# Performance work log

Measured on AMD Instinct MI355X. Metric: run time of the kernel, lower is better.

## Reference

```python
import jax, jax.numpy as jnp
import numpy as np

N_NODES = 10000
N_EDGES = 128000


def _edge_conv(x, row, col, edge_attr, w1, b1, w2, b2):
    # gather endpoints, concat edge features, 2-layer MLP per edge
    m = jnp.concatenate([x[row], x[col], edge_attr], axis=1)  # [E, 2*in+edge]
    m = jax.nn.relu(m @ w1 + b1) @ w2 + b2                    # [E, out]
    # scatter-mean onto source nodes (flow='target_to_source' -> aggregate on row)
    n = x.shape[0]
    s = jax.ops.segment_sum(m, row, num_segments=n)
    cnt = jax.ops.segment_sum(jnp.ones((row.shape[0], 1), m.dtype), row, num_segments=n)
    out = s / jnp.maximum(cnt, 1.0)
    return out, m


def setup_inputs() -> dict:
    key = jax.random.key(0)
    ks = jax.random.split(key, 24)
    f = jnp.float32

    def lin(kw, kb, fan_in, fan_out):
        lim = 1.0 / np.sqrt(fan_in)
        w = jax.random.uniform(kw, (fan_in, fan_out), f, -lim, lim)
        b = jax.random.uniform(kb, (fan_out,), f, -lim, lim)
        return w, b

    inp = {}
    inp['x_org'] = jax.random.normal(ks[0], (N_NODES, 256), f)
    inp['x_rot'] = jax.random.normal(ks[1], (N_NODES, 4), f)
    inp['edge_index'] = jax.random.randint(ks[2], (2, N_EDGES), 0, N_NODES, jnp.int64 if jax.config.jax_enable_x64 else jnp.int32)
    inp['edge_attr'] = jax.random.normal(ks[3], (N_EDGES, 640), f)
    inp['edge_rot'] = jax.random.normal(ks[4], (N_EDGES, 4), f)

    # conv1: Linear(2*260+644=1164, 64), Linear(64, 64)
    inp['c1_w1'], inp['c1_b1'] = lin(ks[5], ks[6], 1164, 64)
    inp['c1_w2'], inp['c1_b2'] = lin(ks[7], ks[8], 64, 64)
    # conv2: Linear(2*64+704=832, 64), Linear(64, 64)
    inp['c2_w1'], inp['c2_b1'] = lin(ks[9], ks[10], 832, 64)
    inp['c2_w2'], inp['c2_b2'] = lin(ks[11], ks[12], 64, 64)
    # conv3: Linear(2*128+128=384, 64), Linear(64, 64)
    inp['c3_w1'], inp['c3_b1'] = lin(ks[13], ks[14], 384, 64)
    inp['c3_w2'], inp['c3_b2'] = lin(ks[15], ks[16], 64, 64)
    # conv4: Linear(384, 64), Linear(64, 64)
    inp['c4_w1'], inp['c4_b1'] = lin(ks[17], ks[18], 384, 64)
    inp['c4_w2'], inp['c4_b2'] = lin(ks[19], ks[20], 64, 64)
    # lin1: Linear(64, 4)
    inp['lin1_w'], inp['lin1_b'] = lin(ks[21], ks[22], 64, 4)
    # edge_fc: Linear(64, 32) -> ReLU -> Linear(32, 1)
    k23 = jax.random.split(ks[23], 4)
    inp['efc_w1'], inp['efc_b1'] = lin(k23[0], k23[1], 64, 32)
    inp['efc_w2'], inp['efc_b2'] = lin(k23[2], k23[3], 32, 1)
    return inp


def reference(x_org, x_rot, edge_index, edge_attr, edge_rot,
              c1_w1, c1_b1, c1_w2, c1_b2,
              c2_w1, c2_b1, c2_w2, c2_b2,
              c3_w1, c3_b1, c3_w2, c3_b2,
              c4_w1, c4_b1, c4_w2, c4_b2,
              lin1_w, lin1_b, efc_w1, efc_b1, efc_w2, efc_b2):
    node_feat = jnp.concatenate([x_org, x_rot], axis=1)
    edge_feat = jnp.concatenate([edge_attr, edge_rot], axis=1)
    row, col = edge_index[0], edge_index[1]
    E = edge_index.shape[1]

    x1, edge_x1 = _edge_conv(node_feat, row, col, edge_feat, c1_w1, c1_b1, c1_w2, c1_b2)
    edge_x1 = jax.nn.relu(edge_x1)

    x2, edge_x2 = _edge_conv(x1, row, col, jnp.concatenate([edge_attr, edge_x1], axis=1),
                             c2_w1, c2_b1, c2_w2, c2_b2)
    x2 = jax.nn.relu(x2)
    edge_x2 = jax.nn.relu(edge_x2)

    x3, edge_x3 = _edge_conv(jnp.concatenate([x2, x1], axis=1), row, col,
                             jnp.concatenate([edge_x2, edge_x1], axis=1),
                             c3_w1, c3_b1, c3_w2, c3_b2)
    x3 = jax.nn.relu(x3)
    edge_x3 = jax.nn.relu(edge_x3)

    x4, edge_x4 = _edge_conv(jnp.concatenate([x3, x2], axis=1), row, col,
                             jnp.concatenate([edge_x3, edge_x2], axis=1),
                             c4_w1, c4_b1, c4_w2, c4_b2)
    x4 = jax.nn.relu(x4)

    x = x4 @ lin1_w + lin1_b  # [N, 4]
    h = edge_x4[: E // 2] + edge_x4[E // 2:]
    pred_edge_res = jax.nn.relu(h @ efc_w1 + efc_b1) @ efc_w2 + efc_b2  # [E/2, 1]

    # F.normalize(x, p=2, dim=1)
    x = x / jnp.maximum(jnp.linalg.norm(x, axis=1, keepdims=True), 1e-12)
    return x, pred_edge_res
```

## Files before the change

### kernel.cpp

```cpp
#include <hip/hip_runtime.h>
#include <stdint.h>


#define N_NODES 10000
#define N_EDGES 128000
#define E_HALF  64000
#define NBLK    1000

typedef unsigned short u16;

using bf16x8 = __attribute__((ext_vector_type(8))) short;
using f32x4  = __attribute__((ext_vector_type(4))) float;

#define MFMA16(A, B, C) C = __builtin_amdgcn_mfma_f32_16x16x32_bf16(A, B, C, 0, 0, 0)

__device__ __align__(256) float g_acc[N_NODES * 64];
__device__ __align__(256) float g_deg[N_NODES];
__device__ __align__(256) float g_P[N_NODES * 128];
__device__ __align__(256) float g_x1[N_NODES * 64];
__device__ __align__(256) float g_x2[N_NODES * 64];
__device__ __align__(256) float g_x3[N_NODES * 64];
__device__ __align__(256) u16  g_fragA[(size_t)NBLK * 16384];
__device__ __align__(256) u16  g_fragB[(size_t)NBLK * 16384];
__device__ __align__(256) float g_Q2 [(size_t)N_EDGES * 64];
__device__ __align__(256) float g_ex4[(size_t)N_EDGES * 64];
__device__ __align__(256) u16  g_wpA_hi[2 * 4096];
__device__ __align__(256) u16  g_wpA_lo[2 * 4096];
__device__ __align__(256) u16  g_wp2_hi[4096];
__device__ __align__(256) u16  g_wp2_lo[4096];
__device__ __align__(256) u16  g_wnp_hi[4 * 8192];
__device__ __align__(256) u16  g_wnp_lo[4 * 8192];
__device__ __align__(256) u16  g_wpC_hi[10 * 8192];
__device__ __align__(256) u16  g_wpC_lo[10 * 8192];
__device__ __align__(256) int g_row[N_EDGES];
__device__ __align__(256) int g_col[N_EDGES];
__device__ int g_mode;
__device__ int g_is64;

__device__ __forceinline__ float b2f(u16 u) {
    return __uint_as_float(((unsigned int)u) << 16);
}
__device__ __forceinline__ u16 f2b(float f) {
    unsigned int u = __float_as_uint(f);
    u += 0x7FFFu + ((u >> 16) & 1u);
    return (u16)(u >> 16);
}
__device__ __forceinline__ float ldf(const u16* p)   { return b2f(*p); }
__device__ __forceinline__ float ldf(const float* p) { return *p; }
__device__ __forceinline__ void  stf(u16* p, float v)   { *p = f2b(v); }
__device__ __forceinline__ void  stf(float* p, float v) { *p = v; }

__device__ __forceinline__ float4 load4(const float* p) { return *(const float4*)p; }
__device__ __forceinline__ float4 load4(const u16* p) {
    ushort4 v = *(const ushort4*)p;
    return make_float4(b2f(v.x), b2f(v.y), b2f(v.z), b2f(v.w));
}

__device__ __forceinline__ void gl_lds16(const void* g, void* l) {
    __builtin_amdgcn_global_load_lds(
        (const __attribute__((address_space(1))) void*)g,
        (__attribute__((address_space(3))) void*)l, 16, 0, 0);
}

__device__ __forceinline__ void split_pack(float4 v, uint2& hi, uint2& lo) {
    unsigned int ux = __float_as_uint(v.x), uy = __float_as_uint(v.y);
    unsigned int uz = __float_as_uint(v.z), uw = __float_as_uint(v.w);
    unsigned int hx = ux & 0xFFFF0000u, hy = uy & 0xFFFF0000u;
    unsigned int hz = uz & 0xFFFF0000u, hw = uw & 0xFFFF0000u;
    hi.x = (hx >> 16) | hy;
    hi.y = (hz >> 16) | hw;
    u16 lx = f2b(v.x - __uint_as_float(hx));
    u16 ly = f2b(v.y - __uint_as_float(hy));
    u16 lz = f2b(v.z - __uint_as_float(hz));
    u16 lw = f2b(v.w - __uint_as_float(hw));
    lo.x = (unsigned int)lx | ((unsigned int)ly << 16);
    lo.y = (unsigned int)lz | ((unsigned int)lw << 16);
}

__device__ __forceinline__ void mk_frag(float4 v0, float4 v1,
                                        bf16x8& fh, bf16x8& fl) {
    uint2 h0, l0, h1, l1;
    split_pack(v0, h0, l0);
    split_pack(v1, h1, l1);
    union { unsigned int w[4]; bf16x8 v; } H, L;
    H.w[0] = h0.x; H.w[1] = h0.y; H.w[2] = h1.x; H.w[3] = h1.y;
    L.w[0] = l0.x; L.w[1] = l0.y; L.w[2] = l1.x; L.w[3] = l1.y;
    fh = H.v; fl = L.v;
}

__global__ void detect_kernel(const void* x_org_v, const int* __restrict__ eidx) {
    const u16* w = (const u16*)x_org_v;
    const int t = threadIdx.x;
    int ok = 0;
    for (int i = t; i < 128; i += 64) {
        u16 v = w[i];
        int ex = (v >> 7) & 0xFF;
        ok += ((ex >= 0x68 && ex <= 0x88) || ((v & 0x7FFFu) == 0)) ? 1 : 0;
    }
    #pragma unroll
    for (int off = 32; off >= 1; off >>= 1) ok += __shfl_xor(ok, off);
    bool allz = true;
    for (int i = t; i < 2048; i += 64) allz = allz && (eidx[2 * i + 1] == 0);
    unsigned long long m = __ballot(allz);
    if (t == 0) {
        g_mode = (ok >= 110) ? 0 : 1;
        g_is64 = (m == ~0ull) ? 1 : 0;
    }
}

__global__ void cvt_idx(const int* __restrict__ eidx) {
    const int e = blockIdx.x * 256 + threadIdx.x;
    if (g_is64) {
        g_row[e] = eidx[2 * e];
        g_col[e] = eidx[2 * (e + N_EDGES)];
    } else {
        g_row[e] = eidx[e];
        g_col[e] = eidx[e + N_EDGES];
    }
}

__global__ void zero_all() {
    const int i = blockIdx.x * 256 + threadIdx.x;
    g_acc[i] = 0.f;
    if (i < N_NODES) g_deg[i] = 0.f;
}

__global__ void deg_kernel() {
    const int e = blockIdx.x * 256 + threadIdx.x;
    if (e < N_EDGES) atomicAdd(&g_deg[g_row[e]], 1.0f);
}

template<typename TW>
__device__ void pack_w_body(const TW* w1a, const TW* w2, const TW* w1b,
                            int we, int ns, int hioff, int nsn, int nsc) {
    const int idx = blockIdx.x * 256 + threadIdx.x;
    const int t1 = ns * 4096;
    const int t2 = t1 + 4096;
    const int t3 = t2 + nsn * 8192;
    if (idx < t1) {
        const int s = idx >> 12;
        const int rem = idx & 4095;
        const int kt = rem >> 11, ct = (rem >> 9) & 3, l = (rem >> 3) & 63, r = rem & 7;
        const int k = s * 64 + kt * 32 + 4 * (l >> 4) + (r & 3) + 16 * (r >> 2);
        const float v = ldf(w1a + (size_t)(we + k) * 64 + ct * 16 + (l & 15));
        const u16 hh = f2b(v);
        g_wpA_hi[idx] = hh;
        g_wpA_lo[idx] = f2b(v - b2f(hh));
    } else if (idx < t2) {
        const int rem = idx - t1;
        const int kt = rem >> 11, ct = (rem >> 9) & 3, l = (rem >> 3) & 63, r = rem & 7;
        const int k = kt * 32 + 4 * (l >> 4) + (r & 3) + 16 * (r >> 2);
        const float v = ldf(w2 + (size_t)k * 64 + ct * 16 + (l & 15));
        const u16 hh = f2b(v);
        g_wp2_hi[rem] = hh;
        g_wp2_lo[rem] = f2b(v - b2f(hh));
    } else if (idx < t3) {
        const int rem = idx - t2;
        const int s = rem >> 13;
        const int kt = (rem >> 12) & 1, ct = (rem >> 9) & 7, l = (rem >> 3) & 63, r = rem & 7;
        const int k = s * 64 + kt * 32 + 4 * (l >> 4) + (r & 3) + 16 * (r >> 2);
        const int col = ct * 16 + (l & 15);
        const int row = (col < 64) ? k : (hioff + k);
        const float v = ldf(w1a + (size_t)row * 64 + (col & 63));
        const u16 hh = f2b(v);
        g_wnp_hi[rem] = hh;
        g_wnp_lo[rem] = f2b(v - b2f(hh));
    } else if (idx < t3 + nsc * 8192) {
        const int rem = idx - t3;
        const int s = rem >> 13;
        const int kt = (rem >> 12) & 1, ct = (rem >> 9) & 7, l = (rem >> 3) & 63, r = rem & 7;
        const int k = s * 64 + kt * 32 + 4 * (l >> 4) + (r & 3) + 16 * (r >> 2);
        const int col = ct * 16 + (l & 15);
        float v;
        if (col < 64) v = ldf(w1a + (size_t)(520 + k) * 64 + col);
        else          v = ldf(w1b + (size_t)(128 + k) * 64 + (col - 64));
        const u16 hh = f2b(v);
        g_wpC_hi[rem] = hh;
        g_wpC_lo[rem] = f2b(v - b2f(hh));
    }
}
__global__ void pack_w_k(const void* w1a, const void* w2, const void* w1b,
                         int we, int ns, int hioff, int nsn, int nsc) {
    if (g_mode == 0)
        pack_w_body<u16>((const u16*)w1a, (const u16*)w2, (const u16*)w1b,
                         we, ns, hioff, nsn, nsc);
    else
        pack_w_body<float>((const float*)w1a, (const float*)w2, (const float*)w1b,
                         we, ns, hioff, nsn, nsc);
}

template<typename TA, int NS1, int NS2, bool TAIL>
__device__ void node_mfma_body(float* smrot, float* smwt,
        const TA* A1, const float* A2, const TA* rotsrc, const TA* w1, float* P) {
    constexpr int NS = NS1 + NS2;
    const int t = threadIdx.x;
    const int lane = t & 63, wid = t >> 6;
    const int q = lane >> 4, n = lane & 15;
    const int r0b = blockIdx.x * 64;

    if constexpr (TAIL) {
        if (t < 64) {
            const int rr = min(r0b + t, N_NODES - 1);
            float4 v = load4(rotsrc + (size_t)rr * 4);
            smrot[t * 4 + 0] = v.x; smrot[t * 4 + 1] = v.y;
            smrot[t * 4 + 2] = v.z; smrot[t * 4 + 3] = v.w;
        }
        for (int i = t; i < 512; i += 256) {
            const int j = i >> 7, c = i & 127;
            const int row = (c < 64) ? (256 + j) : (516 + j);
            smwt[i] = ldf(w1 + (size_t)row * 64 + (c & 63));
        }
        __syncthreads();
    }

    const int arow = min(r0b + wid * 16 + n, N_NODES - 1);

    f32x4 acc[8];
    #pragma unroll
    for (int ct = 0; ct < 8; ++ct) acc[ct] = (f32x4){0.f, 0.f, 0.f, 0.f};

    #pragma unroll
    for (int s = 0; s < NS; ++s) {
        #pragma unroll
        for (int kt = 0; kt < 2; ++kt) {
            float4 v0, v1;
            if (s < NS1) {
                const TA* p = A1 + (size_t)arow * (NS1 * 64) + s * 64 + kt * 32 + q * 4;
                v0 = load4(p); v1 = load4(p + 16);
            } else {
                const float* p = A2 + (size_t)arow * (NS2 * 64) + (s - NS1) * 64
                               + kt * 32 + q * 4;
                v0 = load4(p); v1 = load4(p + 16);
            }
            bf16x8 ah, al;
            mk_frag(v0, v1, ah, al);
            const u16* wph = g_wnp_hi + s * 8192;
            const u16* wpl = g_wnp_lo + s * 8192;
            #pragma unroll
            for (int ct = 0; ct < 8; ++ct) {
                bf16x8 bh = *(const bf16x8*)&wph[(kt * 8 + ct) * 512 + lane * 8];
                bf16x8 bl = *(const bf16x8*)&wpl[(kt * 8 + ct) * 512 + lane * 8];
                MFMA16(ah, bh, acc[ct]);
                MFMA16(al, bh, acc[ct]);
                MFMA16(ah, bl, acc[ct]);
            }
        }
    }

    #pragma unroll
    for (int ct = 0; ct < 8; ++ct) {
        #pragma unroll
        for (int i = 0; i < 4; ++i) {
            const int rl = wid * 16 + 4 * q + i;
            const int row = r0b + rl;
            const int col = ct * 16 + n;
            float v = acc[ct][i];
            if constexpr (TAIL)
                v += smrot[rl * 4 + 0] * smwt[0 * 128 + col]
                   + smrot[rl * 4 + 1] * smwt[1 * 128 + col]
                   + smrot[rl * 4 + 2] * smwt[2 * 128 + col]
                   + smrot[rl * 4 + 3] * smwt[3 * 128 + col];
            if (row < N_NODES) P[(size_t)row * 128 + col] = v;
        }
    }
}

template<int NS1, bool TAIL>
__global__ void __launch_bounds__(256) node_mfma_in(
        const void* A1, const void* rotsrc, const void* w1, float* __restrict__ P) {
    __shared__ float smrot[256], smwt[512];
    if (g_mode == 0)
        node_mfma_body<u16, NS1, 0, TAIL>(smrot, smwt, (const u16*)A1,
            nullptr, (const u16*)rotsrc, (const u16*)w1, P);
    else
        node_mfma_body<float, NS1, 0, TAIL>(smrot, smwt, (const float*)A1,
            nullptr, (const float*)rotsrc, (const float*)w1, P);
}

template<int NS1, int NS2>
__global__ void __launch_bounds__(256) node_mfma_ws(
        const float* A1, const float* A2, float* __restrict__ P) {
    __shared__ float smrot[256], smwt[512];
    node_mfma_body<float, NS1, NS2, false>(smrot, smwt, A1, A2,
        (const float*)nullptr, (const float*)nullptr, P);
}

__device__ __forceinline__ void frag_store_o(u16* hreg, int wid, int lane,
        const f32x4 (&oacc)[2][4], u16* Fdst, int blkid) {
    const int q = lane >> 4, n = lane & 15;
    #pragma unroll
    for (int rt = 0; rt < 2; ++rt)
        #pragma unroll
        for (int ct = 0; ct < 4; ++ct)
            #pragma unroll
            for (int i = 0; i < 4; ++i) {
                float v = fmaxf(oacc[rt][ct][i], 0.f);
                unsigned int hb = __float_as_uint(v) & 0xFFFF0000u;
                const u16 hh = (u16)(hb >> 16);
                const u16 hl = f2b(v - __uint_as_float(hb));
                const int off = wid * 4096
                              + (((ct >> 1) * 2 + rt) * 64 + (n >> 2) * 16 + 4 * q + i) * 8
                              + (ct & 1) * 4 + (n & 3);
                hreg[off]        = hh;
                hreg[off + 2048] = hl;
            }
    #pragma unroll
    for (int kt = 0; kt < 2; ++kt)
        #pragma unroll
        for (int rtl = 0; rtl < 2; ++rtl) {
            const int src = wid * 4096 + ((kt * 2 + rtl) * 64 + lane) * 8;
            bf16x8 h8 = *(const bf16x8*)&hreg[src];
            bf16x8 l8 = *(const bf16x8*)&hreg[src + 2048];
            const size_t gb = (size_t)blkid * 16384
                            + (size_t)(kt * 8 + wid * 2 + rtl) * 512 + lane * 8;
            *(bf16x8*)&Fdst[gb]        = h8;
            *(bf16x8*)&Fdst[gb + 8192] = l8;
        }
}

template<typename TA, typename TW>
__device__ void edge_c1_body(u16* smW, int* srow, int* scol,
        float* b1s, float* b2s, float* rot, float* wtl,
        const TA* efa, const TA* rotsrc,
        const TW* w1, const TW* b1v, const TW* b2v) {
    const int t = threadIdx.x;
    const int lane = t & 63, wid = t >> 6;
    const int q = lane >> 4, n = lane & 15;
    const int e0 = blockIdx.x * 128;

    if (t < 128) srow[t] = g_row[e0 + t];
    else         scol[t - 128] = g_col[e0 + t - 128];
    if (t >= 128 && t < 192) b1s[t - 128] = ldf(b1v + (t - 128));
    if (t >= 192)            b2s[t - 192] = ldf(b2v + (t - 192));
    if (t < 128) {
        float4 r4 = load4(rotsrc + (size_t)(e0 + t) * 4);
        rot[t * 4 + 0] = r4.x; rot[t * 4 + 1] = r4.y;
        rot[t * 4 + 2] = r4.z; rot[t * 4 + 3] = r4.w;
    }
    wtl[t] = ldf(w1 + (size_t)(1160 + (t >> 6)) * 64 + (t & 63));

    const TA* arow0 = efa + (size_t)(e0 + wid * 32 + n) * 640;
    const TA* arow1 = efa + (size_t)(e0 + wid * 32 + 16 + n) * 640;

    f32x4 acc[2][8];
    #pragma unroll
    for (int a_ = 0; a_ < 2; ++a_)
        #pragma unroll
        for (int b_ = 0; b_ < 8; ++b_)
            acc[a_][b_] = (f32x4){0.f, 0.f, 0.f, 0.f};

    auto stageW = [&](int s) {
        const char* srch = (const char*)g_wpC_hi + (size_t)s * 16384;
        const char* srcl = (const char*)g_wpC_lo + (size_t)s * 16384;
        char* dsth = (char*)smW + (size_t)(s & 1) * 32768;
        char* dstl = dsth + 16384;
        #pragma unroll
        for (int i = 0; i < 4; ++i) {
            const int off = wid * 4096 + i * 1024;
            gl_lds16(srch + off + lane * 16, dsth + off);
            gl_lds16(srcl + off + lane * 16, dstl + off);
        }
    };
    auto stageW2 = [&]() {
        #pragma unroll
        for (int i = 0; i < 4; ++i) {
            const int L = wid * 4096 + i * 1024;
            const char* src = (L < 8192) ? (const char*)g_wp2_hi + L
// ... 78 lines not shown
                        + g_P[(size_t)srow[rl] * 128 + col]
                        + g_P[(size_t)scol[rl] * 128 + 64 + col]
                        + rot[rl * 4 + 0] * wtl[0 * 64 + col]
                        + rot[rl * 4 + 1] * wtl[1 * 64 + col]
                        + rot[rl * 4 + 2] * wtl[2 * 64 + col]
                        + rot[rl * 4 + 3] * wtl[3 * 64 + col];
                v = fmaxf(v, 0.f);
                unsigned int hb = __float_as_uint(v) & 0xFFFF0000u;
                const u16 hh = (u16)(hb >> 16);
                const u16 hl = f2b(v - __uint_as_float(hb));
                const int off = wid * 4096
                              + (((ct >> 1) * 2 + rt) * 64 + (n >> 2) * 16 + 4 * q + i) * 8
                              + (ct & 1) * 4 + (n & 3);
                hreg[off]        = hh;
                hreg[off + 2048] = hl;
            }

    __builtin_amdgcn_sched_barrier(0);
    asm volatile("s_waitcnt vmcnt(0)");
    __builtin_amdgcn_sched_barrier(0);
    __builtin_amdgcn_s_barrier();

    f32x4 oacc[2][4];
    #pragma unroll
    for (int rt = 0; rt < 2; ++rt)
        #pragma unroll
        for (int ct = 0; ct < 4; ++ct) {
            const float bb = b2s[ct * 16 + n];
            oacc[rt][ct] = (f32x4){bb, bb, bb, bb};
        }
    #pragma unroll
    for (int kt = 0; kt < 2; ++kt) {
        const int r0 = wid * 4096 + ((kt * 2 + 0) * 64 + lane) * 8;
        const int r1 = wid * 4096 + ((kt * 2 + 1) * 64 + lane) * 8;
        bf16x8 ah0 = *(const bf16x8*)&hreg[r0];
        bf16x8 ah1 = *(const bf16x8*)&hreg[r1];
        bf16x8 al0 = *(const bf16x8*)&hreg[r0 + 2048];
        bf16x8 al1 = *(const bf16x8*)&hreg[r1 + 2048];
        #pragma unroll
        for (int ct = 0; ct < 4; ++ct) {
            bf16x8 bh = *(const bf16x8*)&smW[(kt * 4 + ct) * 512 + lane * 8];
            bf16x8 bl = *(const bf16x8*)&smW[4096 + (kt * 4 + ct) * 512 + lane * 8];
            MFMA16(ah0, bh, oacc[0][ct]);
            MFMA16(ah1, bh, oacc[1][ct]);
            MFMA16(al0, bh, oacc[0][ct]);
            MFMA16(al1, bh, oacc[1][ct]);
            MFMA16(ah0, bl, oacc[0][ct]);
            MFMA16(ah1, bl, oacc[1][ct]);
        }
    }

    #pragma unroll
    for (int rt = 0; rt < 2; ++rt)
        #pragma unroll
        for (int ct = 0; ct < 4; ++ct)
            #pragma unroll
            for (int i = 0; i < 4; ++i) {
                const int rl = wid * 32 + rt * 16 + 4 * q + i;
                atomicAdd(&g_acc[(size_t)srow[rl] * 64 + ct * 16 + n], oacc[rt][ct][i]);
            }
    frag_store_o(hreg, wid, lane, oacc, g_fragA, blockIdx.x);
}

__global__ void __launch_bounds__(256, 2) edge_c1(
        const void* efa, const void* rotsrc,
        const void* w1, const void* b1, const void* b2) {
    __shared__ __align__(16) u16 smW[32768];
    __shared__ int srow[128], scol[128];
    __shared__ float b1s[64], b2s[64], rot[512], wtl[256];
    if (g_mode == 0)
        edge_c1_body<u16, u16>(smW, srow, scol, b1s, b2s, rot, wtl,
            (const u16*)efa, (const u16*)rotsrc,
            (const u16*)w1, (const u16*)b1, (const u16*)b2);
    else
        edge_c1_body<float, float>(smW, srow, scol, b1s, b2s, rot, wtl,
            (const float*)efa, (const float*)rotsrc,
            (const float*)w1, (const float*)b1, (const float*)b2);
}

template<typename TW, int NSF, bool HASQ2, bool FRAG_OUT>
__device__ void edge_lite_body(u16* smW, int* srow, int* scol,
        float* b1s, float* b2s,
        const u16* f0, const u16* f1,
        const TW* b1v, const TW* b2v, u16* Ffrag, float* fout) {
    const int t = threadIdx.x;
    const int lane = t & 63, wid = t >> 6;
    const int q = lane >> 4, n = lane & 15;
    const int e0 = blockIdx.x * 128;
    const size_t blkb = (size_t)blockIdx.x * 16384;
    constexpr int N2 = 2 * NSF * 4096;

    #pragma unroll
    for (int i = 0; i < (NSF + 1) * 4; ++i) {
        const int L = wid * ((NSF + 1) * 4096) + i * 1024;
        const char* src;
        if (L < NSF * 8192)                 src = (const char*)g_wpA_hi + L;
        else if (L < 2 * NSF * 8192)        src = (const char*)g_wpA_lo + (L - NSF * 8192);
        else if (L < 2 * NSF * 8192 + 8192) src = (const char*)g_wp2_hi + (L - 2 * NSF * 8192);
        else                                src = (const char*)g_wp2_lo + (L - 2 * NSF * 8192 - 8192);
        gl_lds16(src + lane * 16, (char*)smW + L);
    }

    if (t < 128) srow[t] = g_row[e0 + t];
    else         scol[t - 128] = g_col[e0 + t - 128];
    if (t >= 128 && t < 192) b1s[t - 128] = ldf(b1v + (t - 128));
    if (t >= 192)            b2s[t - 192] = ldf(b2v + (t - 192));
    __syncthreads();

    f32x4 acc[2][4];
    #pragma unroll
    for (int a_ = 0; a_ < 2; ++a_)
        #pragma unroll
        for (int b_ = 0; b_ < 4; ++b_)
            acc[a_][b_] = (f32x4){0.f, 0.f, 0.f, 0.f};

    #pragma unroll
    for (int s = 0; s < NSF; ++s) {
        const u16* fs = (s == 0) ? f0 : f1;
        #pragma unroll
        for (int kt = 0; kt < 2; ++kt) {
            const size_t ba0 = blkb + (size_t)(kt * 8 + wid * 2 + 0) * 512 + lane * 8;
            const size_t ba1 = blkb + (size_t)(kt * 8 + wid * 2 + 1) * 512 + lane * 8;
            bf16x8 ah0 = *(const bf16x8*)&fs[ba0];
            bf16x8 al0 = *(const bf16x8*)&fs[ba0 + 8192];
            bf16x8 ah1 = *(const bf16x8*)&fs[ba1];
            bf16x8 al1 = *(const bf16x8*)&fs[ba1 + 8192];
            #pragma unroll
            for (int ct = 0; ct < 4; ++ct) {
                bf16x8 bh = *(const bf16x8*)&smW[s * 4096 + (kt * 4 + ct) * 512 + lane * 8];
                bf16x8 bl = *(const bf16x8*)&smW[NSF * 4096 + s * 4096 + (kt * 4 + ct) * 512 + lane * 8];
                MFMA16(ah0, bh, acc[0][ct]);
                MFMA16(ah1, bh, acc[1][ct]);
                MFMA16(al0, bh, acc[0][ct]);
                MFMA16(al1, bh, acc[1][ct]);
                MFMA16(ah0, bl, acc[0][ct]);
                MFMA16(ah1, bl, acc[1][ct]);
            }
        }
    }

    __builtin_amdgcn_s_barrier();
    u16* hreg = smW + (NSF == 1 ? 16384 : 0);

    #pragma unroll
    for (int rt = 0; rt < 2; ++rt)
        #pragma unroll
        for (int ct = 0; ct < 4; ++ct)
            #pragma unroll
            for (int i = 0; i < 4; ++i) {
                const int rl = wid * 32 + rt * 16 + 4 * q + i;
                const int col = ct * 16 + n;
                float v = acc[rt][ct][i] + b1s[col]
                        + g_P[(size_t)srow[rl] * 128 + col]
                        + g_P[(size_t)scol[rl] * 128 + 64 + col];
                if constexpr (HASQ2)
                    v += g_Q2[(size_t)(e0 + rl) * 64 + col];
                v = fmaxf(v, 0.f);
                unsigned int hb = __float_as_uint(v) & 0xFFFF0000u;
                const u16 hh = (u16)(hb >> 16);
                const u16 hl = f2b(v - __uint_as_float(hb));
                const int off = wid * 4096
                              + (((ct >> 1) * 2 + rt) * 64 + (n >> 2) * 16 + 4 * q + i) * 8
                              + (ct & 1) * 4 + (n & 3);
                hreg[off]        = hh;
                hreg[off + 2048] = hl;
            }

    f32x4 oacc[2][4];
    #pragma unroll
    for (int rt = 0; rt < 2; ++rt)
        #pragma unroll
        for (int ct = 0; ct < 4; ++ct) {
            const float bb = b2s[ct * 16 + n];
            oacc[rt][ct] = (f32x4){bb, bb, bb, bb};
        }
    #pragma unroll
    for (int kt = 0; kt < 2; ++kt) {
        const int r0 = wid * 4096 + ((kt * 2 + 0) * 64 + lane) * 8;
        const int r1 = wid * 4096 + ((kt * 2 + 1) * 64 + lane) * 8;
        bf16x8 ah0 = *(const bf16x8*)&hreg[r0];
        bf16x8 ah1 = *(const bf16x8*)&hreg[r1];
        bf16x8 al0 = *(const bf16x8*)&hreg[r0 + 2048];
        bf16x8 al1 = *(const bf16x8*)&hreg[r1 + 2048];
        #pragma unroll
        for (int ct = 0; ct < 4; ++ct) {
            bf16x8 bh = *(const bf16x8*)&smW[N2 + (kt * 4 + ct) * 512 + lane * 8];
            bf16x8 bl = *(const bf16x8*)&smW[N2 + 4096 + (kt * 4 + ct) * 512 + lane * 8];
            MFMA16(ah0, bh, oacc[0][ct]);
            MFMA16(ah1, bh, oacc[1][ct]);
            MFMA16(al0, bh, oacc[0][ct]);
            MFMA16(al1, bh, oacc[1][ct]);
            MFMA16(ah0, bl, oacc[0][ct]);
            MFMA16(ah1, bl, oacc[1][ct]);
        }
    }

    #pragma unroll
    for (int rt = 0; rt < 2; ++rt)
        #pragma unroll
        for (int ct = 0; ct < 4; ++ct)
            #pragma unroll
            for (int i = 0; i < 4; ++i) {
                const int rl = wid * 32 + rt * 16 + 4 * q + i;
                const int col = ct * 16 + n;
                const float v = oacc[rt][ct][i];
                atomicAdd(&g_acc[(size_t)srow[rl] * 64 + col], v);
                if constexpr (!FRAG_OUT)
                    fout[(size_t)(e0 + rl) * 64 + col] = v;
            }
    if constexpr (FRAG_OUT)
        frag_store_o(hreg, wid, lane, oacc, Ffrag, blockIdx.x);
}

template<int NSF, bool HASQ2, bool FRAG_OUT>
__global__ void __launch_bounds__(256, 2) edge_lite(
        const u16* f0, const u16* f1, const void* b1, const void* b2,
        u16* Ffrag, float* fout) {
    __shared__ __align__(16) u16 smW[(NSF == 1) ? 32768 : 24576];
    __shared__ int srow[128], scol[128];
    __shared__ float b1s[64], b2s[64];
    if (g_mode == 0)
        edge_lite_body<u16, NSF, HASQ2, FRAG_OUT>(smW, srow, scol, b1s, b2s,
            f0, f1, (const u16*)b1, (const u16*)b2, Ffrag, fout);
    else
        edge_lite_body<float, NSF, HASQ2, FRAG_OUT>(smW, srow, scol, b1s, b2s,
            f0, f1, (const float*)b1, (const float*)b2, Ffrag, fout);
}

template<bool RELU>
__global__ void finalize_k(float* __restrict__ dst) {
    const int idx = blockIdx.x * 256 + threadIdx.x;
    float v = g_acc[idx] / fmaxf(g_deg[idx >> 6], 1.0f);
    g_acc[idx] = 0.f;
    if (RELU) v = fmaxf(v, 0.f);
    dst[idx] = v;
}

template<typename T>
__device__ void final_node_body(const T* w, const T* b, T* out) {
    const int t = threadIdx.x;
    const int lane = t & 63;
    const int n = blockIdx.x * 4 + (t >> 6);
    float inv = 1.0f / fmaxf(g_deg[n], 1.0f);
    float x4 = fmaxf(g_acc[(size_t)n * 64 + lane] * inv, 0.0f);
    float r[4];
    #pragma unroll
    for (int j = 0; j < 4; ++j) {
        float v = x4 * ldf(w + lane * 4 + j);
        #pragma unroll
        for (int off = 32; off >= 1; off >>= 1) v += __shfl_xor(v, off);
        r[j] = v + ldf(b + j);
    }
    float nrm = sqrtf(r[0]*r[0] + r[1]*r[1] + r[2]*r[2] + r[3]*r[3]);
    float dn = fmaxf(nrm, 1e-12f);
    if (lane < 4) stf(out + n * 4 + lane, r[lane] / dn);
}
__global__ void final_node(const void* w, const void* b, void* out) {
    if (g_mode == 0) final_node_body<u16>((const u16*)w, (const u16*)b, (u16*)out);
    else             final_node_body<float>((const float*)w, (const float*)b, (float*)out);
}

template<typename T>
__device__ void edge_head_body(const float* ex4, const T* w1, const T* b1,
                               const T* w2, const T* b2, T* out) {
    __shared__ float lw1[2048];
    __shared__ float lw2[32];
    const int t = threadIdx.x;
    for (int i = t; i < 2048; i += 256) lw1[i] = ldf(w1 + i);
    if (t < 32) lw2[t] = ldf(w2 + t);
    __syncthreads();
    const int e = blockIdx.x * 256 + t;
    float a[32];
    #pragma unroll
    for (int j = 0; j < 32; ++j) a[j] = ldf(b1 + j);
    const float* p0 = ex4 + (size_t)e * 64;
    const float* p1 = ex4 + (size_t)(e + E_HALF) * 64;
    for (int c = 0; c < 64; ++c) {
        float h = p0[c] + p1[c];
        #pragma unroll
        for (int j = 0; j < 32; ++j) a[j] += h * lw1[c * 32 + j];
    }
    float s = ldf(b2);
    #pragma unroll
    for (int j = 0; j < 32; ++j) s += fmaxf(a[j], 0.f) * lw2[j];
    stf(out + e, s);
}
__global__ void __launch_bounds__(256) edge_head(const float* ex4,
        const void* w1, const void* b1, const void* w2, const void* b2,
        void* out) {
    if (g_mode == 0)
        edge_head_body<u16>(ex4, (const u16*)w1, (const u16*)b1,
                            (const u16*)w2, (const u16*)b2, (u16*)out + 40000);
    else
        edge_head_body<float>(ex4, (const float*)w1, (const float*)b1,
                              (const float*)w2, (const float*)b2, (float*)out + 40000);
}

__global__ void sentinel_fill(unsigned int* out, int n_words) {
    int i = blockIdx.x * 256 + threadIdx.x;
    if (i < n_words) out[i] = 0x44794479u;
}

static void* sym_addr(const void* symbol) {
    void* p = nullptr;
    (void)hipGetSymbolAddress(&p, symbol);
    return p;
}

extern "C" void kernel_launch(void* const* d_in, const int* in_sizes, int n_in,
                              void* d_out, int out_size, void* d_ws, size_t ws_size,
                              hipStream_t stream) {
    (void)d_ws; (void)ws_size;
    bool ok = (n_in == 27) && (out_size == 104000)
           && (in_sizes[0] == 2560000) && (in_sizes[2] == 256000)
           && (in_sizes[3] == 81920000) && (in_sizes[5] == 74496)
           && (in_sizes[21] == 256) && (in_sizes[25] == 32);
    if (!ok) {
        sentinel_fill<<<204, 256, 0, stream>>>((unsigned int*)d_out, 52000);
        return;
    }
    const void* x_org     = d_in[0];
    const void* x_rot     = d_in[1];
    const int*  eidx      = (const int*)d_in[2];
    const void* edge_attr = d_in[3];
    const void* edge_rot  = d_in[4];

    float* P   = (float*)sym_addr(HIP_SYMBOL(g_P));
    float* x1  = (float*)sym_addr(HIP_SYMBOL(g_x1));
    float* x2  = (float*)sym_addr(HIP_SYMBOL(g_x2));
    float* x3  = (float*)sym_addr(HIP_SYMBOL(g_x3));
    u16*   fA  = (u16*)sym_addr(HIP_SYMBOL(g_fragA));
    u16*   fB  = (u16*)sym_addr(HIP_SYMBOL(g_fragB));
    float* ex4 = (float*)sym_addr(HIP_SYMBOL(g_ex4));

    detect_kernel<<<1, 64, 0, stream>>>(x_org, eidx);
    cvt_idx<<<500, 256, 0, stream>>>(eidx);
    zero_all<<<2500, 256, 0, stream>>>();
    deg_kernel<<<500, 256, 0, stream>>>();

    pack_w_k<<<464, 256, 0, stream>>>(d_in[5], d_in[7], d_in[9], 0, 0, 260, 4, 10);
    node_mfma_in<4, true><<<157, 256, 0, stream>>>(x_org, x_rot, d_in[5], P);
    edge_c1<<<NBLK, 256, 0, stream>>>(edge_attr, edge_rot, d_in[5], d_in[6], d_in[8]);
    finalize_k<false><<<2500, 256, 0, stream>>>(x1);

    pack_w_k<<<64, 256, 0, stream>>>(d_in[9], d_in[11], d_in[9], 768, 1, 64, 1, 0);
    node_mfma_ws<1, 0><<<157, 256, 0, stream>>>(x1, nullptr, P);
    edge_lite<1, true, true><<<NBLK, 256, 0, stream>>>(
        fA, nullptr, d_in[10], d_in[12], fB, nullptr);
    finalize_k<true><<<2500, 256, 0, stream>>>(x2);

    pack_w_k<<<112, 256, 0, stream>>>(d_in[13], d_in[15], d_in[13], 256, 2, 128, 2, 0);
    node_mfma_ws<1, 1><<<157, 256, 0, stream>>>(x2, x1, P);
    edge_lite<2, false, true><<<NBLK, 256, 0, stream>>>(
        fB, fA, d_in[14], d_in[16], fA, nullptr);
    finalize_k<true><<<2500, 256, 0, stream>>>(x3);

    pack_w_k<<<112, 256, 0, stream>>>(d_in[17], d_in[19], d_in[17], 256, 2, 128, 2, 0);
    node_mfma_ws<1, 1><<<157, 256, 0, stream>>>(x3, x2, P);
    edge_lite<2, false, false><<<NBLK, 256, 0, stream>>>(
        fA, fB, d_in[18], d_in[20], nullptr, ex4);

    final_node<<<2500, 256, 0, stream>>>(d_in[21], d_in[22], d_out);
    edge_head<<<250, 256, 0, stream>>>(ex4, d_in[23], d_in[24], d_in[25], d_in[26],
                                       d_out);
}
```

Baseline: 843.0 us.

## Fuse prologue, weight packing, finalize and tail kernels to cut launch count

Result: faster. 820.0 us (-2.7%).

```diff
diff --git a/kernel.cpp b/kernel.cpp
--- a/kernel.cpp
+++ b/kernel.cpp
@@ -24,12 +24,12 @@
 __device__ __align__(256) u16  g_fragB[(size_t)NBLK * 16384];
 __device__ __align__(256) float g_Q2 [(size_t)N_EDGES * 64];
 __device__ __align__(256) float g_ex4[(size_t)N_EDGES * 64];
-__device__ __align__(256) u16  g_wpA_hi[2 * 4096];
-__device__ __align__(256) u16  g_wpA_lo[2 * 4096];
-__device__ __align__(256) u16  g_wp2_hi[4096];
-__device__ __align__(256) u16  g_wp2_lo[4096];
-__device__ __align__(256) u16  g_wnp_hi[4 * 8192];
-__device__ __align__(256) u16  g_wnp_lo[4 * 8192];
+__device__ __align__(256) u16  g_wpA_hi[5 * 4096];
+__device__ __align__(256) u16  g_wpA_lo[5 * 4096];
+__device__ __align__(256) u16  g_wp2_hi[4 * 4096];
+__device__ __align__(256) u16  g_wp2_lo[4 * 4096];
+__device__ __align__(256) u16  g_wnp_hi[9 * 8192];
+__device__ __align__(256) u16  g_wnp_lo[9 * 8192];
 __device__ __align__(256) u16  g_wpC_hi[10 * 8192];
 __device__ __align__(256) u16  g_wpC_lo[10 * 8192];
 __device__ __align__(256) int g_row[N_EDGES];
@@ -88,130 +88,124 @@
     fh = H.v; fl = L.v;
 }
 
-__global__ void detect_kernel(const void* x_org_v, const int* __restrict__ eidx) {
-    const u16* w = (const u16*)x_org_v;
-    const int t = threadIdx.x;
-    int ok = 0;
-    for (int i = t; i < 128; i += 64) {
-        u16 v = w[i];
-        int ex = (v >> 7) & 0xFF;
-        ok += ((ex >= 0x68 && ex <= 0x88) || ((v & 0x7FFFu) == 0)) ? 1 : 0;
-    }
-    #pragma unroll
-    for (int off = 32; off >= 1; off >>= 1) ok += __shfl_xor(ok, off);
-    bool allz = true;
-    for (int i = t; i < 2048; i += 64) allz = allz && (eidx[2 * i + 1] == 0);
-    unsigned long long m = __ballot(allz);
-    if (t == 0) {
-        g_mode = (ok >= 110) ? 0 : 1;
-        g_is64 = (m == ~0ull) ? 1 : 0;
-    }
-}
-
-__global__ void cvt_idx(const int* __restrict__ eidx) {
-    const int e = blockIdx.x * 256 + threadIdx.x;
-    if (g_is64) {
-        g_row[e] = eidx[2 * e];
-        g_col[e] = eidx[2 * (e + N_EDGES)];
-    } else {
-        g_row[e] = eidx[e];
-        g_col[e] = eidx[e + N_EDGES];
-    }
-}
-
-__global__ void zero_all() {
+__global__ void prologue_a(const void* x_org_v, const int* __restrict__ eidx) {
     const int i = blockIdx.x * 256 + threadIdx.x;
     g_acc[i] = 0.f;
     if (i < N_NODES) g_deg[i] = 0.f;
-}
-
-__global__ void deg_kernel() {
-    const int e = blockIdx.x * 256 + threadIdx.x;
-    if (e < N_EDGES) atomicAdd(&g_deg[g_row[e]], 1.0f);
-}
-
+    if (blockIdx.x == 0 && threadIdx.x < 64) {
+        const u16* w = (const u16*)x_org_v;
+        const int t = threadIdx.x;
+        int ok = 0;
+        for (int j = t; j < 128; j += 64) {
+            u16 v = w[j];
+            int ex = (v >> 7) & 0xFF;
+            ok += ((ex >= 0x68 && ex <= 0x88) || ((v & 0x7FFFu) == 0)) ? 1 : 0;
+        }
+        #pragma unroll
+        for (int off = 32; off >= 1; off >>= 1) ok += __shfl_xor(ok, off);
+        bool allz = true;
+        for (int j = t; j < 2048; j += 64) allz = allz && (eidx[2 * j + 1] == 0);
+        unsigned long long m = __ballot(allz);
+        if (t == 0) {
+            g_mode = (ok >= 110) ? 0 : 1;
+            g_is64 = (m == ~0ull) ? 1 : 0;
+        }
+    }
+}
+
+__device__ __forceinline__ void pack_pair(u16* dh, u16* dl, float v) {
+    const u16 hh = f2b(v);
+    *dh = hh; *dl = f2b(v - b2f(hh));
+}
 template<typename TW>
-__device__ void pack_w_body(const TW* w1a, const TW* w2, const TW* w1b,
-                            int we, int ns, int hioff, int nsn, int nsc) {
+__device__ void pack_wnp(const TW* w, int hioff, int rem, u16* dh, u16* dl) {
+    const int s = rem >> 13, kt = (rem >> 12) & 1, ct = (rem >> 9) & 7,
+              l = (rem >> 3) & 63, r = rem & 7;
+    const int k = s * 64 + kt * 32 + 4 * (l >> 4) + (r & 3) + 16 * (r >> 2);
+    const int col = ct * 16 + (l & 15);
+    const int row = (col < 64) ? k : (hioff + k);
+    pack_pair(dh + rem, dl + rem, ldf(w + (size_t)row * 64 + (col & 63)));
+}
+template<typename TW>
+__device__ void pack_wpa(const TW* w, int we, int rem, u16* dh, u16* dl) {
+    const int s = rem >> 12, kt = (rem >> 11) & 1, ct = (rem >> 9) & 3,
+              l = (rem >> 3) & 63, r = rem & 7;
+    const int k = s * 64 + kt * 32 + 4 * (l >> 4) + (r & 3) + 16 * (r >> 2);
+    pack_pair(dh + rem, dl + rem,
+              ldf(w + (size_t)(we + k) * 64 + ct * 16 + (l & 15)));
+}
+template<typename TW>
+__device__ void pack_wpc(const TW* w1, const TW* w2w, int rem) {
+    const int s = rem >> 13, kt = (rem >> 12) & 1, ct = (rem >> 9) & 7,
+              l = (rem >> 3) & 63, r = rem & 7;
+    const int k = s * 64 + kt * 32 + 4 * (l >> 4) + (r & 3) + 16 * (r >> 2);
+    const int col = ct * 16 + (l & 15);
+    float v = (col < 64) ? ldf(w1 + (size_t)(520 + k) * 64 + col)
+                         : ldf(w2w + (size_t)(128 + k) * 64 + (col - 64));
+    pack_pair(g_wpC_hi + rem, g_wpC_lo + rem, v);
+}
+
+template<typename TW>
+__device__ void pack_all_body(const TW* c1w1, const TW* c1w2, const TW* c2w1,
+        const TW* c2w2, const TW* c3w1, const TW* c3w2, const TW* c4w1,
+        const TW* c4w2) {
     const int idx = blockIdx.x * 256 + threadIdx.x;
-    const int t1 = ns * 4096;
-    const int t2 = t1 + 4096;
-    const int t3 = t2 + nsn * 8192;
-    if (idx < t1) {
-        const int s = idx >> 12;
-        const int rem = idx & 4095;
-        const int kt = rem >> 11, ct = (rem >> 9) & 3, l = (rem >> 3) & 63, r = rem & 7;
-        const int k = s * 64 + kt * 32 + 4 * (l >> 4) + (r & 3) + 16 * (r >> 2);
-        const float v = ldf(w1a + (size_t)(we + k) * 64 + ct * 16 + (l & 15));
-        const u16 hh = f2b(v);
-        g_wpA_hi[idx] = hh;
-        g_wpA_lo[idx] = f2b(v - b2f(hh));
-    } else if (idx < t2) {
-        const int rem = idx - t1;
-        const int kt = rem >> 11, ct = (rem >> 9) & 3, l = (rem >> 3) & 63, r = rem & 7;
-        const int k = kt * 32 + 4 * (l >> 4) + (r & 3) + 16 * (r >> 2);
-        const float v = ldf(w2 + (size_t)k * 64 + ct * 16 + (l & 15));
-        const u16 hh = f2b(v);
-        g_wp2_hi[rem] = hh;
-        g_wp2_lo[rem] = f2b(v - b2f(hh));
-    } else if (idx < t3) {
-        const int rem = idx - t2;
-        const int s = rem >> 13;
-        const int kt = (rem >> 12) & 1, ct = (rem >> 9) & 7, l = (rem >> 3) & 63, r = rem & 7;
-        const int k = s * 64 + kt * 32 + 4 * (l >> 4) + (r & 3) + 16 * (r >> 2);
-        const int col = ct * 16 + (l & 15);
-        const int row = (col < 64) ? k : (hioff + k);
-        const float v = ldf(w1a + (size_t)row * 64 + (col & 63));
-        const u16 hh = f2b(v);
-        g_wnp_hi[rem] = hh;
-        g_wnp_lo[rem] = f2b(v - b2f(hh));
-    } else if (idx < t3 + nsc * 8192) {
-        const int rem = idx - t3;
-        const int s = rem >> 13;
-        const int kt = (rem >> 12) & 1, ct = (rem >> 9) & 7, l = (rem >> 3) & 63, r = rem & 7;
-        const int k = s * 64 + kt * 32 + 4 * (l >> 4) + (r & 3) + 16 * (r >> 2);
-        const int col = ct * 16 + (l & 15);
-        float v;
-        if (col < 64) v = ldf(w1a + (size_t)(520 + k) * 64 + col);
-        else          v = ldf(w1b + (size_t)(128 + k) * 64 + (col - 64));
-        const u16 hh = f2b(v);
-        g_wpC_hi[rem] = hh;
-        g_wpC_lo[rem] = f2b(v - b2f(hh));
-    }
-}
-__global__ void pack_w_k(const void* w1a, const void* w2, const void* w1b,
-                         int we, int ns, int hioff, int nsn, int nsc) {
-    if (g_mode == 0)
-        pack_w_body<u16>((const u16*)w1a, (const u16*)w2, (const u16*)w1b,
-                         we, ns, hioff, nsn, nsc);
-    else
-        pack_w_body<float>((const float*)w1a, (const float*)w2, (const float*)w1b,
-                         we, ns, hioff, nsn, nsc);
-}
-
-template<typename TA, int NS1, int NS2, bool TAIL>
-__device__ void node_mfma_body(float* smrot, float* smwt,
-        const TA* A1, const float* A2, const TA* rotsrc, const TA* w1, float* P) {
-    constexpr int NS = NS1 + NS2;
+    if (idx < 81920)        pack_wpc<TW>(c1w1, c2w1, idx);
+    else if (idx < 114688)  pack_wnp<TW>(c1w1, 260, idx - 81920,  g_wnp_hi,            g_wnp_lo);
+    else if (idx < 122880)  pack_wnp<TW>(c2w1, 64,  idx - 114688, g_wnp_hi + 4 * 8192, g_wnp_lo + 4 * 8192);
+    else if (idx < 139264)  pack_wnp<TW>(c3w1, 128, idx - 122880, g_wnp_hi + 5 * 8192, g_wnp_lo + 5 * 8192);
+    else if (idx < 155648)  pack_wnp<TW>(c4w1, 128, idx - 139264, g_wnp_hi + 7 * 8192, g_wnp_lo + 7 * 8192);
+    else if (idx < 159744)  pack_wpa<TW>(c2w1, 768, idx - 155648, g_wpA_hi,            g_wpA_lo);
+    else if (idx < 167936)  pack_wpa<TW>(c3w1, 256, idx - 159744, g_wpA_hi + 4096,     g_wpA_lo + 4096);
+    else if (idx < 176128)  pack_wpa<TW>(c4w1, 256, idx - 167936, g_wpA_hi + 12288,    g_wpA_lo + 12288);
+    else if (idx < 180224)  pack_wpa<TW>(c1w2, 0,   idx - 176128, g_wp2_hi,            g_wp2_lo);
+    else if (idx < 184320)  pack_wpa<TW>(c2w2, 0,   idx - 180224, g_wp2_hi + 4096,     g_wp2_lo + 4096);
+    else if (idx < 188416)  pack_wpa<TW>(c3w2, 0,   idx - 184320, g_wp2_hi + 8192,     g_wp2_lo + 8192);
+    else if (idx < 192512)  pack_wpa<TW>(c4w2, 0,   idx - 188416, g_wp2_hi + 12288,    g_wp2_lo + 12288);
+}
+
+__global__ void prep_k(const void* c1w1, const void* c1w2, const void* c2w1,
+        const void* c2w2, const void* c3w1, const void* c3w2, const void* c4w1,
+        const void* c4w2, const int* __restrict__ eidx) {
+    if ((int)blockIdx.x < 752) {
+        if (g_mode == 0)
+            pack_all_body<u16>((const u16*)c1w1, (const u16*)c1w2, (const u16*)c2w1,
+                (const u16*)c2w2, (const u16*)c3w1, (const u16*)c3w2,
+                (const u16*)c4w1, (const u16*)c4w2);
+        else
+            pack_all_body<float>((const float*)c1w1, (const float*)c1w2,
+                (const float*)c2w1, (const float*)c2w2, (const float*)c3w1,
+                (const float*)c3w2, (const float*)c4w1, (const float*)c4w2);
+    } else {
+        const int e = ((int)blockIdx.x - 752) * 256 + threadIdx.x;
+        int row, col;
+        if (g_is64) { row = eidx[2 * e]; col = eidx[2 * (e + N_EDGES)]; }
+        else        { row = eidx[e];     col = eidx[e + N_EDGES]; }
+        g_row[e] = row; g_col[e] = col;
+        atomicAdd(&g_deg[row], 1.0f);
+    }
+}
+
+template<typename TA>
+__device__ void node_mfma_in_body(float* smrot, float* smwt,
+        const TA* A1, const TA* rotsrc, const TA* w1, float* P) {
     const int t = threadIdx.x;
     const int lane = t & 63, wid = t >> 6;
     const int q = lane >> 4, n = lane & 15;
     const int r0b = blockIdx.x * 64;
 
-    if constexpr (TAIL) {
-        if (t < 64) {
-            const int rr = min(r0b + t, N_NODES - 1);
-            float4 v = load4(rotsrc + (size_t)rr * 4);
-            smrot[t * 4 + 0] = v.x; smrot[t * 4 + 1] = v.y;
-            smrot[t * 4 + 2] = v.z; smrot[t * 4 + 3] = v.w;
-        }
-        for (int i = t; i < 512; i += 256) {
-            const int j = i >> 7, c = i & 127;
-            const int row = (c < 64) ? (256 + j) : (516 + j);
-            smwt[i] = ldf(w1 + (size_t)row * 64 + (c & 63));
-        }
-        __syncthreads();
-    }
+    if (t < 64) {
+        const int rr = min(r0b + t, N_NODES - 1);
+        float4 v = load4(rotsrc + (size_t)rr * 4);
+        smrot[t * 4 + 0] = v.x; smrot[t * 4 + 1] = v.y;
+        smrot[t * 4 + 2] = v.z; smrot[t * 4 + 3] = v.w;
+    }
+    for (int i = t; i < 512; i += 256) {
+        const int j = i >> 7, c = i & 127;
+        const int row = (c < 64) ? (256 + j) : (516 + j);
+        smwt[i] = ldf(w1 + (size_t)row * 64 + (c & 63));
+    }
+    __syncthreads();
 
     const int arow = min(r0b + wid * 16 + n, N_NODES - 1);
 
@@ -220,18 +214,11 @@
     for (int ct = 0; ct < 8; ++ct) acc[ct] = (f32x4){0.f, 0.f, 0.f, 0.f};
 
     #pragma unroll
-    for (int s = 0; s < NS; ++s) {
+    for (int s = 0; s < 4; ++s) {
         #pragma unroll
         for (int kt = 0; kt < 2; ++kt) {
-            float4 v0, v1;
-            if (s < NS1) {
-                const TA* p = A1 + (size_t)arow * (NS1 * 64) + s * 64 + kt * 32 + q * 4;
-                v0 = load4(p); v1 = load4(p + 16);
-            } else {
-                const float* p = A2 + (size_t)arow * (NS2 * 64) + (s - NS1) * 64
-                               + kt * 32 + q * 4;
-                v0 = load4(p); v1 = load4(p + 16);
-            }
+            const TA* p = A1 + (size_t)arow * 256 + s * 64 + kt * 32 + q * 4;
+            float4 v0 = load4(p), v1 = load4(p + 16);
             bf16x8 ah, al;
             mk_frag(v0, v1, ah, al);
             const u16* wph = g_wnp_hi + s * 8192;
@@ -254,35 +241,104 @@
             const int rl = wid * 16 + 4 * q + i;
             const int row = r0b + rl;
             const int col = ct * 16 + n;
-            float v = acc[ct][i];
-            if constexpr (TAIL)
-                v += smrot[rl * 4 + 0] * smwt[0 * 128 + col]
-                   + smrot[rl * 4 + 1] * smwt[1 * 128 + col]
-                   + smrot[rl * 4 + 2] * smwt[2 * 128 + col]
-                   + smrot[rl * 4 + 3] * smwt[3 * 128 + col];
+            float v = acc[ct][i]
+                    + smrot[rl * 4 + 0] * smwt[0 * 128 + col]
+                    + smrot[rl * 4 + 1] * smwt[1 * 128 + col]
+                    + smrot[rl * 4 + 2] * smwt[2 * 128 + col]
+                    + smrot[rl * 4 + 3] * smwt[3 * 128 + col];
             if (row < N_NODES) P[(size_t)row * 128 + col] = v;
         }
     }
 }
 
-template<int NS1, bool TAIL>
 __global__ void __launch_bounds__(256) node_mfma_in(
         const void* A1, const void* rotsrc, const void* w1, float* __restrict__ P) {
     __shared__ float smrot[256], smwt[512];
     if (g_mode == 0)
-        node_mfma_body<u16, NS1, 0, TAIL>(smrot, smwt, (const u16*)A1,
-            nullptr, (const u16*)rotsrc, (const u16*)w1, P);
+        node_mfma_in_body<u16>(smrot, smwt, (const u16*)A1, (const u16*)rotsrc,
+                               (const u16*)w1, P);
     else
-        node_mfma_body<float, NS1, 0, TAIL>(smrot, smwt, (const float*)A1,
-            nullptr, (const float*)rotsrc, (const float*)w1, P);
-}
-
-template<int NS1, int NS2>
-__global__ void __launch_bounds__(256) node_mfma_ws(
-        const float* A1, const float* A2, float* __restrict__ P) {
-    __shared__ float smrot[256], smwt[512];
-    node_mfma_body<float, NS1, NS2, false>(smrot, smwt, A1, A2,
-        (const float*)nullptr, (const float*)nullptr, P);
+        node_mfma_in_body<float>(smrot, smwt, (const float*)A1, (const float*)rotsrc,
+                               (const float*)w1, P);
+}
+
+template<int NS2, bool RELU>
+__global__ void __launch_bounds__(256) node_mfma_acc(
+        const float* A2, float* __restrict__ xout, float* __restrict__ P,
+        int wnpoff) {
+    const int t = threadIdx.x;
+    const int lane = t & 63, wid = t >> 6;
+    const int q = lane >> 4, n = lane & 15;
+    const int r0b = blockIdx.x * 64;
+    const int rown = r0b + wid * 16 + n;
+    const int arow = min(rown, N_NODES - 1);
+    const bool own = rown < N_NODES;
+    const float inv = 1.0f / fmaxf(g_deg[arow], 1.0f);
+
+    f32x4 acc[8];
+    #pragma unroll
+    for (int ct = 0; ct < 8; ++ct) acc[ct] = (f32x4){0.f, 0.f, 0.f, 0.f};
+
+    #pragma unroll
+    for (int kt = 0; kt < 2; ++kt) {
+        float* p = g_acc + (size_t)arow * 64 + kt * 32 + q * 4;
+        float4 v0 = load4(p), v1 = load4(p + 16);
+        v0.x *= inv; v0.y *= inv; v0.z *= inv; v0.w *= inv;
+        v1.x *= inv; v1.y *= inv; v1.z *= inv; v1.w *= inv;
+        if (RELU) {
+            v0.x = fmaxf(v0.x, 0.f); v0.y = fmaxf(v0.y, 0.f);
+            v0.z = fmaxf(v0.z, 0.f); v0.w = fmaxf(v0.w, 0.f);
+            v1.x = fmaxf(v1.x, 0.f); v1.y = fmaxf(v1.y, 0.f);
+            v1.z = fmaxf(v1.z, 0.f); v1.w = fmaxf(v1.w, 0.f);
+        }
+        if (own) {
+            *(float4*)(xout + (size_t)arow * 64 + kt * 32 + q * 4) = v0;
+            *(float4*)(xout + (size_t)arow * 64 + kt * 32 + q * 4 + 16) = v1;
+            *(float4*)p = make_float4(0.f, 0.f, 0.f, 0.f);
+            *(float4*)(p + 16) = make_float4(0.f, 0.f, 0.f, 0.f);
+        }
+        bf16x8 ah, al;
+        mk_frag(v0, v1, ah, al);
+        const u16* wph = g_wnp_hi + wnpoff;
+        const u16* wpl = g_wnp_lo + wnpoff;
+        #pragma unroll
+        for (int ct = 0; ct < 8; ++ct) {
+            bf16x8 bh = *(const bf16x8*)&wph[(kt * 8 + ct) * 512 + lane * 8];
+            bf16x8 bl = *(const bf16x8*)&wpl[(kt * 8 + ct) * 512 + lane * 8];
+            MFMA16(ah, bh, acc[ct]);
+            MFMA16(al, bh, acc[ct]);
+            MFMA16(ah, bl, acc[ct]);
+        }
+    }
+    if constexpr (NS2 > 0) {
+        #pragma unroll
+        for (int kt = 0; kt < 2; ++kt) {
+            const float* p = A2 + (size_t)arow * 64 + kt * 32 + q * 4;
+            float4 v0 = load4(p), v1 = load4(p + 16);
+            bf16x8 ah, al;
+            mk_frag(v0, v1, ah, al);
+            const u16* wph = g_wnp_hi + wnpoff + 8192;
+            const u16* wpl = g_wnp_lo + wnpoff + 8192;
+            #pragma unroll
+            for (int ct = 0; ct < 8; ++ct) {
+                bf16x8 bh = *(const bf16x8*)&wph[(kt * 8 + ct) * 512 + lane * 8];
+                bf16x8 bl = *(const bf16x8*)&wpl[(kt * 8 + ct) * 512 + lane * 8];
+                MFMA16(ah, bh, acc[ct]);
+                MFMA16(al, bh, acc[ct]);
+                MFMA16(ah, bl, acc[ct]);
+            }
+        }
+    }
+
+    #pragma unroll
+    for (int ct = 0; ct < 8; ++ct) {
+        #pragma unroll
+        for (int i = 0; i < 4; ++i) {
+            const int rl = wid * 16 + 4 * q + i;
+            const int row = r0b + rl;
+            if (row < N_NODES) P[(size_t)row * 128 + ct * 16 + n] = acc[ct][i];
+        }
+    }
 }
 
 __device__ __forceinline__ void frag_store_o(u16* hreg, int wid, int lane,
@@ -527,7 +583,8 @@
 __device__ void edge_lite_body(u16* smW, int* srow, int* scol,
         float* b1s, float* b2s,
         const u16* f0, const u16* f1,
-        const TW* b1v, const TW* b2v, u16* Ffrag, float* fout) {
+        const TW* b1v, const TW* b2v, u16* Ffrag, float* fout,
+        int wpAoff, int wp2off) {
     const int t = threadIdx.x;
     const int lane = t & 63, wid = t >> 6;
     const int q = lane >> 4, n = lane & 15;
@@ -539,10 +596,10 @@
     for (int i = 0; i < (NSF + 1) * 4; ++i) {
         const int L = wid * ((NSF + 1) * 4096) + i * 1024;
         const char* src;
-        if (L < NSF * 8192)                 src = (const char*)g_wpA_hi + L;
-        else if (L < 2 * NSF * 8192)        src = (const char*)g_wpA_lo + (L - NSF * 8192);
-        else if (L < 2 * NSF * 8192 + 8192) src = (const char*)g_wp2_hi + (L - 2 * NSF * 8192);
-        else                                src = (const char*)g_wp2_lo + (L - 2 * NSF * 8192 - 8192);
+        if (L < NSF * 8192)                 src = (const char*)(g_wpA_hi + wpAoff) + L;
+        else if (L < 2 * NSF * 8192)        src = (const char*)(g_wpA_lo + wpAoff) + (L - NSF * 8192);
+        else if (L < 2 * NSF * 8192 + 8192) src = (const char*)(g_wp2_hi + wp2off) + (L - 2 * NSF * 8192);
+        else                                src = (const char*)(g_wp2_lo + wp2off) + (L - 2 * NSF * 8192 - 8192);
         gl_lds16(src + lane * 16, (char*)smW + L);
     }
 
@@ -660,32 +717,23 @@
 template<int NSF, bool HASQ2, bool FRAG_OUT>
 __global__ void __launch_bounds__(256, 2) edge_lite(
         const u16* f0, const u16* f1, const void* b1, const void* b2,
-        u16* Ffrag, float* fout) {
+        u16* Ffrag, float* fout, int wpAoff, int wp2off) {
     __shared__ __align__(16) u16 smW[(NSF == 1) ? 32768 : 24576];
     __shared__ int srow[128], scol[128];
     __shared__ float b1s[64], b2s[64];
     if (g_mode == 0)
         edge_lite_body<u16, NSF, HASQ2, FRAG_OUT>(smW, srow, scol, b1s, b2s,
-            f0, f1, (const u16*)b1, (const u16*)b2, Ffrag, fout);
+            f0, f1, (const u16*)b1, (const u16*)b2, Ffrag, fout, wpAoff, wp2off);
     else
         edge_lite_body<float, NSF, HASQ2, FRAG_OUT>(smW, srow, scol, b1s, b2s,
-            f0, f1, (const float*)b1, (const float*)b2, Ffrag, fout);
-}
-
-template<bool RELU>
-__global__ void finalize_k(float* __restrict__ dst) {
-    const int idx = blockIdx.x * 256 + threadIdx.x;
-    float v = g_acc[idx] / fmaxf(g_deg[idx >> 6], 1.0f);
-    g_acc[idx] = 0.f;
-    if (RELU) v = fmaxf(v, 0.f);
-    dst[idx] = v;
+            f0, f1, (const float*)b1, (const float*)b2, Ffrag, fout, wpAoff, wp2off);
 }
 
 template<typename T>
-__device__ void final_node_body(const T* w, const T* b, T* out) {
+__device__ void final_node_body(const T* w, const T* b, T* out, int bid) {
     const int t = threadIdx.x;
     const int lane = t & 63;
-    const int n = blockIdx.x * 4 + (t >> 6);
+    const int n = bid * 4 + (t >> 6);
     float inv = 1.0f / fmaxf(g_deg[n], 1.0f);
     float x4 = fmaxf(g_acc[(size_t)n * 64 + lane] * inv, 0.0f);
     float r[4];
@@ -700,21 +748,17 @@
     float dn = fmaxf(nrm, 1e-12f);
     if (lane < 4) stf(out + n * 4 + lane, r[lane] / dn);
 }
-__global__ void final_node(const void* w, const void* b, void* out) {
-    if (g_mode == 0) final_node_body<u16>((const u16*)w, (const u16*)b, (u16*)out);
-    else             final_node_body<float>((const float*)w, (const float*)b, (float*)out);
-}
 
 template<typename T>
 __device__ void edge_head_body(const float* ex4, const T* w1, const T* b1,
-                               const T* w2, const T* b2, T* out) {
+                               const T* w2, const T* b2, T* out, int bid) {
     __shared__ float lw1[2048];
     __shared__ float lw2[32];
     const int t = threadIdx.x;
     for (int i = t; i < 2048; i += 256) lw1[i] = ldf(w1 + i);
     if (t < 32) lw2[t] = ldf(w2 + t);
     __syncthreads();
-    const int e = blockIdx.x * 256 + t;
+    const int e = bid * 256 + t;
     float a[32];
     #pragma unroll
     for (int j = 0; j < 32; ++j) a[j] = ldf(b1 + j);
@@ -730,15 +774,23 @@
     for (int j = 0; j < 32; ++j) s += fmaxf(a[j], 0.f) * lw2[j];
     stf(out + e, s);
 }
-__global__ void __launch_bounds__(256) edge_head(const float* ex4,
-        const void* w1, const void* b1, const void* w2, const void* b2,
+
+__global__ void __launch_bounds__(256) tail_k(
+        const void* lw, const void* lb, const float* ex4,
+        const void* ew1, const void* eb1, const void* ew2, const void* eb2,
         void* out) {
-    if (g_mode == 0)
-        edge_head_body<u16>(ex4, (const u16*)w1, (const u16*)b1,
-                            (const u16*)w2, (const u16*)b2, (u16*)out + 40000);
-    else
-        edge_head_body<float>(ex4, (const float*)w1, (const float*)b1,
-                              (const float*)w2, (const float*)b2, (float*)out + 40000);
+    const int b = blockIdx.x;
+    if (b < 2500) {
+        if (g_mode == 0) final_node_body<u16>((const u16*)lw, (const u16*)lb, (u16*)out, b);
+        else             final_node_body<float>((const float*)lw, (const float*)lb, (float*)out, b);
+    } else {
+        if (g_mode == 0)
+            edge_head_body<u16>(ex4, (const u16*)ew1, (const u16*)eb1,
+                (const u16*)ew2, (const u16*)eb2, (u16*)out + 40000, b - 2500);
+        else
+            edge_head_body<float>(ex4, (const float*)ew1, (const float*)eb1,
+                (const float*)ew2, (const float*)eb2, (float*)out + 40000, b - 2500);
+    }
 }
 
 __global__ void sentinel_fill(unsigned int* out, int n_words) {
@@ -778,34 +830,25 @@
     u16*   fB  = (u16*)sym_addr(HIP_SYMBOL(g_fragB));
     float* ex4 = (float*)sym_addr(HIP_SYMBOL(g_ex4));
 
-    detect_kernel<<<1, 64, 0, stream>>>(x_org, eidx);
-    cvt_idx<<<500, 256, 0, stream>>>(eidx);
-    zero_all<<<2500, 256, 0, stream>>>();
-    deg_kernel<<<500, 256, 0, stream>>>();
-
-    pack_w_k<<<464, 256, 0, stream>>>(d_in[5], d_in[7], d_in[9], 0, 0, 260, 4, 10);
-    node_mfma_in<4, true><<<157, 256, 0, stream>>>(x_org, x_rot, d_in[5], P);
+    prologue_a<<<2500, 256, 0, stream>>>(x_org, eidx);
+    prep_k<<<1252, 256, 0, stream>>>(d_in[5], d_in[7], d_in[9], d_in[11],
+                                     d_in[13], d_in[15], d_in[17], d_in[19], eidx);
+
+    node_mfma_in<<<157, 256, 0, stream>>>(x_org, x_rot, d_in[5], P);
     edge_c1<<<NBLK, 256, 0, stream>>>(edge_attr, edge_rot, d_in[5], d_in[6], d_in[8]);
-    finalize_k<false><<<2500, 256, 0, stream>>>(x1);
-
-    pack_w_k<<<64, 256, 0, stream>>>(d_in[9], d_in[11], d_in[9], 768, 1, 64, 1, 0);
-    node_mfma_ws<1, 0><<<157, 256, 0, stream>>>(x1, nullptr, P);
+
+    node_mfma_acc<0, false><<<157, 256, 0, stream>>>(nullptr, x1, P, 4 * 8192);
     edge_lite<1, true, true><<<NBLK, 256, 0, stream>>>(
-        fA, nullptr, d_in[10], d_in[12], fB, nullptr);
-    finalize_k<true><<<2500, 256, 0, stream>>>(x2);
-
-    pack_w_k<<<112, 256, 0, stream>>>(d_in[13], d_in[15], d_in[13], 256, 2, 128, 2, 0);
-    node_mfma_ws<1, 1><<<157, 256, 0, stream>>>(x2, x1, P);
+        fA, nullptr, d_in[10], d_in[12], fB, nullptr, 0, 4096);
+
+    node_mfma_acc<1, true><<<157, 256, 0, stream>>>(x1, x2, P, 5 * 8192);
     edge_lite<2, false, true><<<NBLK, 256, 0, stream>>>(
-        fB, fA, d_in[14], d_in[16], fA, nullptr);
-    finalize_k<true><<<2500, 256, 0, stream>>>(x3);
-
-    pack_w_k<<<112, 256, 0, stream>>>(d_in[17], d_in[19], d_in[17], 256, 2, 128, 2, 0);
-    node_mfma_ws<1, 1><<<157, 256, 0, stream>>>(x3, x2, P);
+        fB, fA, d_in[14], d_in[16], fA, nullptr, 4096, 8192);
+
+    node_mfma_acc<1, true><<<157, 256, 0, stream>>>(x2, x3, P, 7 * 8192);
     edge_lite<2, false, false><<<NBLK, 256, 0, stream>>>(
-        fA, fB, d_in[18], d_in[20], nullptr, ex4);
-
-    final_node<<<2500, 256, 0, stream>>>(d_in[21], d_in[22], d_out);
-    edge_head<<<250, 256, 0, stream>>>(ex4, d_in[23], d_in[24], d_in[25], d_in[26],
-                                       d_out);
-}
+        fA, fB, d_in[18], d_in[20], nullptr, ex4, 12288, 12288);
+
+    tail_k<<<2750, 256, 0, stream>>>(d_in[21], d_in[22], ex4,
+                                     d_in[23], d_in[24], d_in[25], d_in[26], d_out);
+}
```
